# Optimization experiments

Hardware: AMD Instinct MI355X
Metric: run time of the kernel (lower is better)

## Reference

```python
import jax, jax.numpy as jnp
import numpy as np

NUM_USERS = 100000
NUM_ITEMS = 50000
NUM_NODES = NUM_USERS + NUM_ITEMS
EMBED_DIM = 128
NUM_LAYERS = 3
CONTENT_DIM = 768
NUM_EDGES = 1000000
BATCH = 4096
LAMBDA_CONTENT = 0.1
INIT_STD = 0.1


def setup_inputs() -> dict:
    key = jax.random.key(0)
    ks = jax.random.split(key, 9)
    edge_index = jax.random.randint(ks[0], (2, NUM_EDGES), 0, NUM_NODES, dtype=jnp.int64 if jax.config.jax_enable_x64 else jnp.int32)
    edge_weight = jax.random.uniform(ks[1], (NUM_EDGES,), dtype=jnp.float32)
    batch_users = jax.random.randint(ks[2], (BATCH,), 0, NUM_USERS)
    batch_pos_items = jax.random.randint(ks[3], (BATCH,), 0, NUM_ITEMS)
    batch_neg_items = jax.random.randint(ks[4], (BATCH,), 0, NUM_ITEMS)
    item_content = jax.random.normal(ks[5], (NUM_ITEMS, CONTENT_DIM), dtype=jnp.float32)
    user_emb_w = INIT_STD * jax.random.normal(ks[6], (NUM_USERS, EMBED_DIM), dtype=jnp.float32)
    item_emb_w = INIT_STD * jax.random.normal(ks[7], (NUM_ITEMS, EMBED_DIM), dtype=jnp.float32)
    # nn.Linear(item_content_dim, embed_dim, bias=False): weight [embed_dim, content_dim]
    bound = 1.0 / np.sqrt(CONTENT_DIM)
    content_proj_w = jax.random.uniform(ks[8], (EMBED_DIM, CONTENT_DIM), minval=-bound, maxval=bound, dtype=jnp.float32)
    return {
        'edge_index': edge_index, 'edge_weight': edge_weight,
        'batch_users': batch_users, 'batch_pos_items': batch_pos_items,
        'batch_neg_items': batch_neg_items, 'item_content': item_content,
        'user_emb_w': user_emb_w, 'item_emb_w': item_emb_w,
        'content_proj_w': content_proj_w,
    }


def _lgconv(x, src, dst, ew, num_nodes):
    # PyG LGConv: gcn_norm(add_self_loops=False) then scatter-add at target.
    deg = jax.ops.segment_sum(ew, dst, num_segments=num_nodes)          # [N]
    dinv = jnp.where(deg > 0, jax.lax.rsqrt(deg), 0.0)
    norm = dinv[src] * ew * dinv[dst]                                    # [E]
    return jax.ops.segment_sum(norm[:, None] * x[src], dst, num_segments=num_nodes)


def _propagate(user_emb_w, item_emb_w, src, dst, ew):
    x = jnp.concatenate([user_emb_w, item_emb_w], axis=0)               # [N, D]
    acc = x
    for _ in range(NUM_LAYERS):
        x = _lgconv(x, src, dst, ew, NUM_NODES)
        acc = acc + x
    x_final = acc / (NUM_LAYERS + 1)
    return x_final[:NUM_USERS], x_final[NUM_USERS:]


def reference(edge_index, edge_weight, batch_users, batch_pos_items,
              batch_neg_items, item_content, user_emb_w, item_emb_w,
              content_proj_w):
    src, dst = edge_index[0], edge_index[1]
    u_final, i_final = _propagate(user_emb_w, item_emb_w, src, dst, edge_weight)
    u = u_final[batch_users]
    i_pos = i_final[batch_pos_items]
    i_neg = i_final[batch_neg_items]
    pos_score = jnp.sum(u * i_pos, axis=-1)
    neg_score = jnp.sum(u * i_neg, axis=-1)
    bpr = jnp.mean(jax.nn.softplus(-(pos_score - neg_score)))
    reg = jnp.mean(jnp.sum(u**2, axis=1) + jnp.sum(i_pos**2, axis=1) + jnp.sum(i_neg**2, axis=1)) * 1e-4
    proj = item_content @ content_proj_w.T                              # [I, D]
    align = jnp.mean((i_final - proj) ** 2)
    loss = bpr + reg + LAMBDA_CONTENT * align
    return loss, u_final, i_final
```

## Files before the change

### kernel.cpp

```cpp
#include <hip/hip_runtime.h>
#include <math.h>

#define NU 100000
#define NI 50000
#define NN 150000
#define D 128
#define NE 1000000
#define CD 768
#define BATCH 4096

typedef short bf16x8 __attribute__((ext_vector_type(8)));
typedef float f32x4 __attribute__((ext_vector_type(4)));

static inline size_t alignup(size_t x, size_t a) { return (x + a - 1) / a * a; }

__device__ inline unsigned short f2bf(float f) {
  unsigned int u = __builtin_bit_cast(unsigned int, f);
  unsigned int r = (u + 0x7fffu + ((u >> 16) & 1u)) >> 16;
  return (unsigned short)r;
}
__device__ inline unsigned int pack2bf(float lo, float hi) {
  return (unsigned int)f2bf(lo) | ((unsigned int)f2bf(hi) << 16);
}
__device__ inline float bflo(unsigned int p) {
  return __builtin_bit_cast(float, p << 16);
}
__device__ inline float bfhi(unsigned int p) {
  return __builtin_bit_cast(float, p & 0xffff0000u);
}

__global__ __launch_bounds__(256) void prep_kernel(
    const int* __restrict__ dst, int* __restrict__ cnt, int* __restrict__ cpos,
    const float* __restrict__ uemb, const float* __restrict__ iemb,
    unsigned int* __restrict__ x0b,
    const float* __restrict__ W, unsigned short* __restrict__ Wb) {
  int half = blockIdx.x >> 1;
  if ((blockIdx.x & 1) == 0) {
    int i = half * 256 + threadIdx.x;
    for (; i < NE; i += 2048 * 256)
      cpos[i] = atomicAdd(&cnt[dst[i]], 1);
  } else {
    const size_t XT = (size_t)NN * D / 8;
    const size_t WT = (size_t)D * CD / 8;
    size_t t = (size_t)half * 256 + threadIdx.x;
    for (; t < XT + WT; t += (size_t)2048 * 256) {
      if (t < XT) {
        size_t f = t * 8;
        const float* p = (f < (size_t)NU * D) ? (uemb + f) : (iemb + (f - (size_t)NU * D));
        float4 a = *(const float4*)p;
        float4 b = *(const float4*)(p + 4);
        uint4 o;
        o.x = pack2bf(a.x, a.y); o.y = pack2bf(a.z, a.w);
        o.z = pack2bf(b.x, b.y); o.w = pack2bf(b.z, b.w);
        *(uint4*)(x0b + t * 4) = o;
      } else {
        size_t f = (t - XT) * 8;
        float4 a = *(const float4*)(W + f);
        float4 b = *(const float4*)(W + f + 4);
        uint4 o;
        o.x = (unsigned int)f2bf(a.x) | ((unsigned int)f2bf(a.y) << 16);
        o.y = (unsigned int)f2bf(a.z) | ((unsigned int)f2bf(a.w) << 16);
        o.z = (unsigned int)f2bf(b.x) | ((unsigned int)f2bf(b.y) << 16);
        o.w = (unsigned int)f2bf(b.z) | ((unsigned int)f2bf(b.w) << 16);
        *(uint4*)(Wb + f) = o;
      }
    }
  }
}


__global__ void scan_p1(const int* __restrict__ cnt, int* __restrict__ bsum) {
  __shared__ int s[256];
  int b = blockIdx.x;
  int i = b * 256 + threadIdx.x;
  s[threadIdx.x] = (i < NN) ? cnt[i] : 0;
  __syncthreads();
  for (int off = 128; off; off >>= 1) {
    if (threadIdx.x < off) s[threadIdx.x] += s[threadIdx.x + off];
    __syncthreads();
  }
  if (threadIdx.x == 0) bsum[b] = s[0];
}

__global__ __launch_bounds__(1024) void scan_p2(int* __restrict__ bsum, int nb) {
  __shared__ int s[1024];
  int t = threadIdx.x;
  int v = (t < nb) ? bsum[t] : 0;
  s[t] = v;
  __syncthreads();
  for (int off = 1; off < 1024; off <<= 1) {
    int u = (t >= off) ? s[t - off] : 0;
    __syncthreads();
    s[t] += u;
    __syncthreads();
  }
  if (t < nb) bsum[t] = s[t] - v;
}

__global__ void scan_p3(const int* __restrict__ cnt, const int* __restrict__ bsum,
                        int* __restrict__ row_ptr) {
  __shared__ int s[256];
  int b = blockIdx.x;
  int i = b * 256 + threadIdx.x;
  s[threadIdx.x] = (i < NN) ? cnt[i] : 0;
  __syncthreads();
  for (int off = 1; off < 256; off <<= 1) {
    int t = (threadIdx.x >= off) ? s[threadIdx.x - off] : 0;
    __syncthreads();
    s[threadIdx.x] += t;
    __syncthreads();
  }
  if (i < NN) row_ptr[i + 1] = bsum[b] + s[threadIdx.x];
  if (i == 0) row_ptr[0] = 0;
}

__global__ void fill_kernel(const int* __restrict__ src, const int* __restrict__ dst,
                            const float* __restrict__ ew, const int* __restrict__ row_ptr,
                            const int* __restrict__ cpos, int* __restrict__ csrc,
                            float* __restrict__ cew) {
  int i = blockIdx.x * blockDim.x + threadIdx.x;
  int stride = gridDim.x * blockDim.x;
  for (; i < NE; i += stride) {
    int p = row_ptr[dst[i]] + cpos[i];
    csrc[p] = src[i];
    cew[p] = ew[i];
  }
}

__global__ void degrow_kernel(const int* __restrict__ row_ptr, const float* __restrict__ cew,
                              float* __restrict__ dinv) {
  int n = blockIdx.x * blockDim.x + threadIdx.x;
  if (n >= NN) return;
  int beg = row_ptr[n], end = row_ptr[n + 1];
  float s = 0.f;
  for (int p = beg; p < end; ++p) s += cew[p];
  dinv[n] = (s > 0.f) ? rsqrtf(s) : 0.f;
}

__global__ void norm_kernel(const int* __restrict__ csrc, const float* __restrict__ cew,
                            const float* __restrict__ dinv, float* __restrict__ cnorm) {
  int i = blockIdx.x * blockDim.x + threadIdx.x;
  int stride = gridDim.x * blockDim.x;
  for (; i < NE; i += stride) cnorm[i] = dinv[csrc[i]] * cew[i];
}

#define GATHER_BODY(SRCBUF)                                                          \
  int tid = threadIdx.x;                                                             \
  int wv = tid >> 6, lane = tid & 63;                                                \
  int g = lane >> 4, sub = lane & 15;                                                \
  int n = blockIdx.x * 16 + wv * 4 + g;                                              \
  if (n >= NN) return;                                                               \
  int beg = row_ptr[n], end = row_ptr[n + 1];                                        \
  float a0 = 0.f, a1 = 0.f, a2 = 0.f, a3 = 0.f, a4 = 0.f, a5 = 0.f, a6 = 0.f, a7 = 0.f; \
  int j = beg;                                                                       \
  for (; j + 2 <= end; j += 2) {                                                     \
    int s0 = csrc[j], s1 = csrc[j + 1];                                              \
    float w0 = cnorm[j], w1 = cnorm[j + 1];                                          \
    uint4 p0 = SRCBUF[(size_t)s0 * 16 + sub];                                        \
    uint4 p1 = SRCBUF[(size_t)s1 * 16 + sub];                                        \
    a0 = fmaf(w0, bflo(p0.x), a0); a1 = fmaf(w0, bfhi(p0.x), a1);                    \
    a2 = fmaf(w0, bflo(p0.y), a2); a3 = fmaf(w0, bfhi(p0.y), a3);                    \
    a4 = fmaf(w0, bflo(p0.z), a4); a5 = fmaf(w0, bfhi(p0.z), a5);                    \
    a6 = fmaf(w0, bflo(p0.w), a6); a7 = fmaf(w0, bfhi(p0.w), a7);                    \
    a0 = fmaf(w1, bflo(p1.x), a0); a1 = fmaf(w1, bfhi(p1.x), a1);                    \
    a2 = fmaf(w1, bflo(p1.y), a2); a3 = fmaf(w1, bfhi(p1.y), a3);                    \
    a4 = fmaf(w1, bflo(p1.z), a4); a5 = fmaf(w1, bfhi(p1.z), a5);                    \
    a6 = fmaf(w1, bflo(p1.w), a6); a7 = fmaf(w1, bfhi(p1.w), a7);                    \
  }                                                                                  \
  if (j < end) {                                                                     \
    int s0 = csrc[j];                                                                \
    float w0 = cnorm[j];                                                             \
    uint4 p0 = SRCBUF[(size_t)s0 * 16 + sub];                                        \
    a0 = fmaf(w0, bflo(p0.x), a0); a1 = fmaf(w0, bfhi(p0.x), a1);                    \
    a2 = fmaf(w0, bflo(p0.y), a2); a3 = fmaf(w0, bfhi(p0.y), a3);                    \
    a4 = fmaf(w0, bflo(p0.z), a4); a5 = fmaf(w0, bfhi(p0.z), a5);                    \
    a6 = fmaf(w0, bflo(p0.w), a6); a7 = fmaf(w0, bfhi(p0.w), a7);                    \
  }

__global__ __launch_bounds__(256) void gather_kernel(
    const int* __restrict__ row_ptr, const int* __restrict__ csrc,
    const float* __restrict__ cnorm, const float* __restrict__ dinv,
    const uint4* __restrict__ xin, uint4* __restrict__ yout) {
  GATHER_BODY(xin)
  float sc = dinv[n];
  uint4 o;
  o.x = pack2bf(a0 * sc, a1 * sc);
  o.y = pack2bf(a2 * sc, a3 * sc);
  o.z = pack2bf(a4 * sc, a5 * sc);
  o.w = pack2bf(a6 * sc, a7 * sc);
  yout[(size_t)n * 16 + sub] = o;
}

__global__ __launch_bounds__(256) void final_kernel(
    const int* __restrict__ row_ptr, const int* __restrict__ csrc,
    const float* __restrict__ cnorm, const float* __restrict__ dinv,
    const uint4* __restrict__ x0b, const uint4* __restrict__ y1b,
    const uint4* __restrict__ y2b, float* __restrict__ OUT) {
  GATHER_BODY(y2b)
  float sc = dinv[n];
  size_t r = (size_t)n * 16 + sub;
  uint4 q0 = x0b[r], q1 = y1b[r], q2 = y2b[r];
  float* op = OUT + (size_t)n * D + sub * 8;
  op[0] = (bflo(q0.x) + bflo(q1.x) + bflo(q2.x) + a0 * sc) * 0.25f;
  op[1] = (bfhi(q0.x) + bfhi(q1.x) + bfhi(q2.x) + a1 * sc) * 0.25f;
  op[2] = (bflo(q0.y) + bflo(q1.y) + bflo(q2.y) + a2 * sc) * 0.25f;
  op[3] = (bfhi(q0.y) + bfhi(q1.y) + bfhi(q2.y) + a3 * sc) * 0.25f;
  op[4] = (bflo(q0.z) + bflo(q1.z) + bflo(q2.z) + a4 * sc) * 0.25f;
  op[5] = (bfhi(q0.z) + bfhi(q1.z) + bfhi(q2.z) + a5 * sc) * 0.25f;
  op[6] = (bflo(q0.w) + bflo(q1.w) + bflo(q2.w) + a6 * sc) * 0.25f;
  op[7] = (bfhi(q0.w) + bfhi(q1.w) + bfhi(q2.w) + a7 * sc) * 0.25f;
}

__global__ __launch_bounds__(512) void align_mfma_kernel(
    const float* __restrict__ content, const unsigned short* __restrict__ Wb,
    const float* __restrict__ ifinal, float* __restrict__ accums) {
  __shared__ unsigned short Asm[2][64 * 64];
  __shared__ unsigned short Bsm[2][128 * 64];
  __shared__ float wred[8];

  int tid = threadIdx.x;
  int w = tid >> 6, lane = tid & 63;
  int i0 = blockIdx.x * 64;
  int lrow = lane & 15, kq = lane >> 4;

  f32x4 acc[4];
#pragma unroll
  for (int rt = 0; rt < 4; ++rt) acc[rt] = (f32x4){0.f, 0.f, 0.f, 0.f};

  int sr = tid >> 3, c8 = tid & 7;
  int arow_g = (i0 + sr < NI) ? (i0 + sr) : (NI - 1);
  const float* aG = content + (size_t)arow_g * CD + c8 * 8;
  const unsigned short* bG0 = Wb + (size_t)sr * CD + c8 * 8;
  const unsigned short* bG1 = Wb + (size_t)(sr + 64) * CD + c8 * 8;
  int aoff = (c8 * 16) ^ ((sr & 7) << 4);
  int boff0 = aoff;
  int boff1 = (c8 * 16) ^ (((sr + 64) & 7) << 4);

  {
    float4 a = *(const float4*)(aG);
    float4 b = *(const float4*)(aG + 4);
    uint4 o;
    o.x = pack2bf(a.x, a.y); o.y = pack2bf(a.z, a.w);
    o.z = pack2bf(b.x, b.y); o.w = pack2bf(b.z, b.w);
    *(uint4*)((char*)Asm[0] + sr * 128 + aoff) = o;
    *(uint4*)((char*)Bsm[0] + sr * 128 + boff0) = *(const uint4*)(bG0);
    *(uint4*)((char*)Bsm[0] + (sr + 64) * 128 + boff1) = *(const uint4*)(bG1);
  }

  for (int kk = 0; kk < 6; ++kk) {
    __syncthreads();
    int cur = kk & 1, nxt = cur ^ 1;
    bool more = kk < 5;
    float4 na, nb;
    uint4 nb0, nb1;
    if (more) {
      int k0 = (kk + 1) * 64;
      na = *(const float4*)(aG + k0);
      nb = *(const float4*)(aG + k0 + 4);
      nb0 = *(const uint4*)(bG0 + k0);
      nb1 = *(const uint4*)(bG1 + k0);
    }
#pragma unroll
    for (int ks = 0; ks < 2; ++ks) {
      int kbyte = ks * 64 + kq * 16;
      bf16x8 af[4], bfr;
#pragma unroll
      for (int rt = 0; rt < 4; ++rt) {
        int row = rt * 16 + lrow;
        af[rt] = *(const bf16x8*)((char*)Asm[cur] + row * 128 + (kbyte ^ ((row & 7) << 4)));
      }
      {
        int row = w * 16 + lrow;
        bfr = *(const bf16x8*)((char*)Bsm[cur] + row * 128 + (kbyte ^ ((row & 7) << 4)));
      }
#pragma unroll
      for (int rt = 0; rt < 4; ++rt)
        acc[rt] = __builtin_amdgcn_mfma_f32_16x16x32_bf16(af[rt], bfr, acc[rt], 0, 0, 0);
    }
    if (more) {
      uint4 o;
      o.x = pack2bf(na.x, na.y); o.y = pack2bf(na.z, na.w);
      o.z = pack2bf(nb.x, nb.y); o.w = pack2bf(nb.z, nb.w);
      *(uint4*)((char*)Asm[nxt] + sr * 128 + aoff) = o;
      *(uint4*)((char*)Bsm[nxt] + sr * 128 + boff0) = nb0;
      *(uint4*)((char*)Bsm[nxt] + (sr + 64) * 128 + boff1) = nb1;
    }
  }

  float s = 0.f;
  int dcol = w * 16 + lrow;
#pragma unroll
  for (int rt = 0; rt < 4; ++rt) {
#pragma unroll
    for (int j = 0; j < 4; ++j) {
      int it = i0 + rt * 16 + kq * 4 + j;
      if (it < NI) {
        float r0 = ifinal[(size_t)it * D + dcol];
        float d0 = r0 - acc[rt][j];
        s = fmaf(d0, d0, s);
      }
    }
  }
  for (int off = 32; off; off >>= 1) s += __shfl_down(s, off);
  if (lane == 0) wred[w] = s;
  __syncthreads();
  if (tid == 0) {
    float t = 0.f;
#pragma unroll
    for (int q = 0; q < 8; ++q) t += wred[q];
    atomicAdd(&accums[2], t);
  }
}

__global__ __launch_bounds__(256) void loss_batch(
    const int* __restrict__ bu, const int* __restrict__ bp, const int* __restrict__ bn,
    const float* __restrict__ OUT, float* __restrict__ accums) {
  __shared__ float wsp[4], wrg[4];
  int wv = threadIdx.x >> 6, lane = threadIdx.x & 63;
  int gw = blockIdx.x * 4 + wv;
  int nw = gridDim.x * 4;
  float lsp = 0.f, lrg = 0.f;
  for (int b = gw; b < BATCH; b += nw) {
    const float* u = OUT + (size_t)bu[b] * D;
    const float* ip = OUT + ((size_t)NU + bp[b]) * D;
    const float* in_ = OUT + ((size_t)NU + bn[b]) * D;
    float u0 = u[lane], u1 = u[lane + 64];
    float p0 = ip[lane], p1 = ip[lane + 64];
    float n0 = in_[lane], n1 = in_[lane + 64];
    float ps = u0 * p0 + u1 * p1;
    float ns = u0 * n0 + u1 * n1;
    float rg = u0 * u0 + u1 * u1 + p0 * p0 + p1 * p1 + n0 * n0 + n1 * n1;
    for (int off = 32; off; off >>= 1) {
      ps += __shfl_down(ps, off);
      ns += __shfl_down(ns, off);
      rg += __shfl_down(rg, off);
    }
    if (lane == 0) {
      float x = ns - ps;
      lsp += fmaxf(x, 0.f) + log1pf(expf(-fabsf(x)));
      lrg += rg;
    }
  }
  if (lane == 0) { wsp[wv] = lsp; wrg[wv] = lrg; }
  __syncthreads();
  if (threadIdx.x == 0) {
    atomicAdd(&accums[0], wsp[0] + wsp[1] + wsp[2] + wsp[3]);
    atomicAdd(&accums[1], wrg[0] + wrg[1] + wrg[2] + wrg[3]);
  }
}

__global__ void finalize_kernel(const float* __restrict__ accums, float* __restrict__ out0) {
  if (threadIdx.x == 0 && blockIdx.x == 0) {
    float bpr = accums[0] / (float)BATCH;
    float reg = (accums[1] / (float)BATCH) * 1e-4f;
    float align = accums[2] / (float)((size_t)NI * D);
    out0[0] = bpr + reg + 0.1f * align;
  }
}

extern "C" void kernel_launch(void* const* d_in, const int* in_sizes, int n_in,
                              void* d_out, int out_size, void* d_ws, size_t ws_size,
                              hipStream_t stream) {
  const int* edge_index = (const int*)d_in[0];
  const float* ew = (const float*)d_in[1];
  const int* bu = (const int*)d_in[2];
  const int* bp = (const int*)d_in[3];
  const int* bn = (const int*)d_in[4];
  const float* content = (const float*)d_in[5];
  const float* uemb = (const float*)d_in[6];
  const float* iemb = (const float*)d_in[7];
  const float* W = (const float*)d_in[8];
  const int* src = edge_index;
  const int* dst = edge_index + NE;
  float* outf = (float*)d_out;
  float* OUT = outf + 1;

  char* ws = (char*)d_ws;
  size_t off = 0;
  auto alloc = [&](size_t bytes) {
    void* p = ws + off;
    off = alignup(off + bytes, 256);
    return p;
  };
  unsigned int* x0b = (unsigned int*)alloc((size_t)NN * 64 * 4);
  unsigned int* y1b = (unsigned int*)alloc((size_t)NN * 64 * 4);
  unsigned int* y2b = (unsigned int*)alloc((size_t)NN * 64 * 4);
  float* dinv = (float*)alloc((size_t)NN * 4);
  int* cnt = (int*)alloc((size_t)NN * 4);
  int* row_ptr = (int*)alloc((size_t)(NN + 1) * 4);
  int NB = (NN + 255) / 256;
  int* bsum = (int*)alloc((size_t)NB * 4);
  int* cpos = (int*)alloc((size_t)NE * 4);
  int* csrc = (int*)alloc((size_t)NE * 4);
  float* cew = (float*)alloc((size_t)NE * 4);
  float* cnorm = (float*)alloc((size_t)NE * 4);
  unsigned short* Wb = (unsigned short*)alloc((size_t)D * CD * 2);
  float* accums = (float*)alloc(16);

  hipMemsetAsync(cnt, 0, (size_t)NN * 4, stream);
  hipMemsetAsync(accums, 0, 16, stream);

  prep_kernel<<<4096, 256, 0, stream>>>(dst, cnt, cpos, uemb, iemb, x0b, W, Wb);
  scan_p1<<<NB, 256, 0, stream>>>(cnt, bsum);
  scan_p2<<<1, 1024, 0, stream>>>(bsum, NB);
  scan_p3<<<NB, 256, 0, stream>>>(cnt, bsum, row_ptr);
  fill_kernel<<<2048, 256, 0, stream>>>(src, dst, ew, row_ptr, cpos, csrc, cew);
  degrow_kernel<<<NB, 256, 0, stream>>>(row_ptr, cew, dinv);
  norm_kernel<<<2048, 256, 0, stream>>>(csrc, cew, dinv, cnorm);

  int LB = (NN + 15) / 16;
  gather_kernel<<<LB, 256, 0, stream>>>(row_ptr, csrc, cnorm, dinv, (const uint4*)x0b, (uint4*)y1b);
  gather_kernel<<<LB, 256, 0, stream>>>(row_ptr, csrc, cnorm, dinv, (const uint4*)y1b, (uint4*)y2b);
  final_kernel<<<LB, 256, 0, stream>>>(row_ptr, csrc, cnorm, dinv,
                                       (const uint4*)x0b, (const uint4*)y1b, (const uint4*)y2b, OUT);

  align_mfma_kernel<<<(NI + 63) / 64, 512, 0, stream>>>(content, Wb, OUT + (size_t)NU * D, accums);
  loss_batch<<<64, 256, 0, stream>>>(bu, bp, bn, OUT, accums);
  finalize_kernel<<<1, 64, 0, stream>>>(accums, outf);
}
```

Before: 341.9 us.

## Fuse content projection GEMM into prep kernel and alignment loss into final gather

Moves the content-projection MFMA GEMM into the prep kernel as extra blocks, so it runs alongside the counting and bf16 conversion work, and writes the projection to a bf16 buffer. The alignment MSE is then computed inside the final gather kernel, which removes the separate align kernel and its re-read of i_final. Partial sums go to 256 slots that a wider finalize kernel reduces. In exchange, the bf16 projection buffer adds a write and read plus extra rounding, and W is now converted to bf16 inside every GEMM block.

```diff
diff --git a/kernel.cpp b/kernel.cpp
--- a/kernel.cpp
+++ b/kernel.cpp
@@ -8,6 +8,7 @@
 #define NE 1000000
 #define CD 768
 #define BATCH 4096
+#define NGEMM 782
 
 typedef short bf16x8 __attribute__((ext_vector_type(8)));
 typedef float f32x4 __attribute__((ext_vector_type(4)));
@@ -29,22 +30,29 @@
   return __builtin_bit_cast(float, p & 0xffff0000u);
 }
 
-__global__ __launch_bounds__(256) void prep_kernel(
+__global__ __launch_bounds__(512) void prep_kernel(
     const int* __restrict__ dst, int* __restrict__ cnt, int* __restrict__ cpos,
     const float* __restrict__ uemb, const float* __restrict__ iemb,
     unsigned int* __restrict__ x0b,
-    const float* __restrict__ W, unsigned short* __restrict__ Wb) {
-  int half = blockIdx.x >> 1;
-  if ((blockIdx.x & 1) == 0) {
-    int i = half * 256 + threadIdx.x;
-    for (; i < NE; i += 2048 * 256)
-      cpos[i] = atomicAdd(&cnt[dst[i]], 1);
-  } else {
-    const size_t XT = (size_t)NN * D / 8;
-    const size_t WT = (size_t)D * CD / 8;
-    size_t t = (size_t)half * 256 + threadIdx.x;
-    for (; t < XT + WT; t += (size_t)2048 * 256) {
-      if (t < XT) {
+    const float* __restrict__ W, const float* __restrict__ content,
+    uint4* __restrict__ proj) {
+  __shared__ unsigned short Asm[2][64 * 64];
+  __shared__ unsigned short Bsm[2][128 * 64];
+
+  int bid = blockIdx.x;
+  int tid = threadIdx.x;
+
+  if (bid >= NGEMM) {
+    int sub = bid - NGEMM;
+    int half = sub >> 1;
+    if ((sub & 1) == 0) {
+      int i = half * 512 + tid;
+      for (; i < NE; i += 1024 * 512)
+        cpos[i] = atomicAdd(&cnt[dst[i]], 1);
+    } else {
+      const size_t XT = (size_t)NN * D / 8;
+      size_t t = (size_t)half * 512 + tid;
+      for (; t < XT; t += (size_t)1024 * 512) {
         size_t f = t * 8;
         const float* p = (f < (size_t)NU * D) ? (uemb + f) : (iemb + (f - (size_t)NU * D));
         float4 a = *(const float4*)p;
@@ -53,18 +61,107 @@
         o.x = pack2bf(a.x, a.y); o.y = pack2bf(a.z, a.w);
         o.z = pack2bf(b.x, b.y); o.w = pack2bf(b.z, b.w);
         *(uint4*)(x0b + t * 4) = o;
-      } else {
-        size_t f = (t - XT) * 8;
-        float4 a = *(const float4*)(W + f);
-        float4 b = *(const float4*)(W + f + 4);
-        uint4 o;
-        o.x = (unsigned int)f2bf(a.x) | ((unsigned int)f2bf(a.y) << 16);
-        o.y = (unsigned int)f2bf(a.z) | ((unsigned int)f2bf(a.w) << 16);
-        o.z = (unsigned int)f2bf(b.x) | ((unsigned int)f2bf(b.y) << 16);
-        o.w = (unsigned int)f2bf(b.z) | ((unsigned int)f2bf(b.w) << 16);
-        *(uint4*)(Wb + f) = o;
       }
     }
+    return;
+  }
+
+  int w = tid >> 6, lane = tid & 63;
+  int i0 = bid * 64;
+  int lrow = lane & 15, kq = lane >> 4;
+
+  f32x4 acc[4];
+#pragma unroll
+  for (int rt = 0; rt < 4; ++rt) acc[rt] = (f32x4){0.f, 0.f, 0.f, 0.f};
+
+  int sr = tid >> 3, c8 = tid & 7;
+  int arow_g = (i0 + sr < NI) ? (i0 + sr) : (NI - 1);
+  const float* aG = content + (size_t)arow_g * CD + c8 * 8;
+  const float* bG0 = W + (size_t)sr * CD + c8 * 8;
+  const float* bG1 = W + (size_t)(sr + 64) * CD + c8 * 8;
+  int aoff = (c8 * 16) ^ ((sr & 7) << 4);
+  int boff0 = aoff;
+  int boff1 = (c8 * 16) ^ (((sr + 64) & 7) << 4);
+
+  {
+    float4 a0 = *(const float4*)(aG);
+    float4 a1 = *(const float4*)(aG + 4);
+    float4 p0 = *(const float4*)(bG0);
+    float4 p1 = *(const float4*)(bG0 + 4);
+    float4 q0 = *(const float4*)(bG1);
+    float4 q1 = *(const float4*)(bG1 + 4);
+    uint4 oa, ob, oc;
+    oa.x = pack2bf(a0.x, a0.y); oa.y = pack2bf(a0.z, a0.w);
+    oa.z = pack2bf(a1.x, a1.y); oa.w = pack2bf(a1.z, a1.w);
+    ob.x = pack2bf(p0.x, p0.y); ob.y = pack2bf(p0.z, p0.w);
+    ob.z = pack2bf(p1.x, p1.y); ob.w = pack2bf(p1.z, p1.w);
+    oc.x = pack2bf(q0.x, q0.y); oc.y = pack2bf(q0.z, q0.w);
+    oc.z = pack2bf(q1.x, q1.y); oc.w = pack2bf(q1.z, q1.w);
+    *(uint4*)((char*)Asm[0] + sr * 128 + aoff) = oa;
+    *(uint4*)((char*)Bsm[0] + sr * 128 + boff0) = ob;
+    *(uint4*)((char*)Bsm[0] + (sr + 64) * 128 + boff1) = oc;
+  }
+
+  for (int kk = 0; kk < 6; ++kk) {
+    __syncthreads();
+    int cur = kk & 1, nxt = cur ^ 1;
+    bool more = kk < 5;
+    float4 a0, a1, p0, p1, q0, q1;
+    if (more) {
+      int k0 = (kk + 1) * 64;
+      a0 = *(const float4*)(aG + k0);
+      a1 = *(const float4*)(aG + k0 + 4);
+      p0 = *(const float4*)(bG0 + k0);
+      p1 = *(const float4*)(bG0 + k0 + 4);
+      q0 = *(const float4*)(bG1 + k0);
+      q1 = *(const float4*)(bG1 + k0 + 4);
+    }
+#pragma unroll
+    for (int ks = 0; ks < 2; ++ks) {
+      int kbyte = ks * 64 + kq * 16;
+      bf16x8 af[4], bfr;
+#pragma unroll
+      for (int rt = 0; rt < 4; ++rt) {
+        int row = rt * 16 + lrow;
+        af[rt] = *(const bf16x8*)((char*)Asm[cur] + row * 128 + (kbyte ^ ((row & 7) << 4)));
+      }
+      {
+        int row = w * 16 + lrow;
+        bfr = *(const bf16x8*)((char*)Bsm[cur] + row * 128 + (kbyte ^ ((row & 7) << 4)));
+      }
+#pragma unroll
+      for (int rt = 0; rt < 4; ++rt)
+        acc[rt] = __builtin_amdgcn_mfma_f32_16x16x32_bf16(af[rt], bfr, acc[rt], 0, 0, 0);
+    }
+    if (more) {
+      uint4 oa, ob, oc;
+      oa.x = pack2bf(a0.x, a0.y); oa.y = pack2bf(a0.z, a0.w);
+      oa.z = pack2bf(a1.x, a1.y); oa.w = pack2bf(a1.z, a1.w);
+      ob.x = pack2bf(p0.x, p0.y); ob.y = pack2bf(p0.z, p0.w);
+      ob.z = pack2bf(p1.x, p1.y); ob.w = pack2bf(p1.z, p1.w);
+      oc.x = pack2bf(q0.x, q0.y); oc.y = pack2bf(q0.z, q0.w);
+      oc.z = pack2bf(q1.x, q1.y); oc.w = pack2bf(q1.z, q1.w);
+      *(uint4*)((char*)Asm[nxt] + sr * 128 + aoff) = oa;
+      *(uint4*)((char*)Bsm[nxt] + sr * 128 + boff0) = ob;
+      *(uint4*)((char*)Bsm[nxt] + (sr + 64) * 128 + boff1) = oc;
+    }
+  }
+
+  __syncthreads();
+  unsigned short* T = (unsigned short*)Asm;
+  int dcol = w * 16 + lrow;
+#pragma unroll
+  for (int rt = 0; rt < 4; ++rt)
+#pragma unroll
+    for (int j = 0; j < 4; ++j)
+      T[(rt * 16 + kq * 4 + j) * 128 + dcol] = f2bf(acc[rt][j]);
+  __syncthreads();
+#pragma unroll
+  for (int u0 = 0; u0 < 2; ++u0) {
+    int u = u0 * 512 + tid;
+    int r = u >> 4, s = u & 15;
+    int it = i0 + r;
+    if (it < NI) proj[(size_t)it * 16 + s] = ((const uint4*)T)[u];
   }
 }
 
@@ -195,120 +292,38 @@
     const int* __restrict__ row_ptr, const int* __restrict__ csrc,
     const float* __restrict__ cnorm, const float* __restrict__ dinv,
     const uint4* __restrict__ x0b, const uint4* __restrict__ y1b,
-    const uint4* __restrict__ y2b, float* __restrict__ OUT) {
+    const uint4* __restrict__ y2b, const uint4* __restrict__ proj,
+    float* __restrict__ OUT, float* __restrict__ partials) {
+  __shared__ float wred[4];
   GATHER_BODY(y2b)
   float sc = dinv[n];
   size_t r = (size_t)n * 16 + sub;
   uint4 q0 = x0b[r], q1 = y1b[r], q2 = y2b[r];
+  float v[8];
+  v[0] = (bflo(q0.x) + bflo(q1.x) + bflo(q2.x) + a0 * sc) * 0.25f;
+  v[1] = (bfhi(q0.x) + bfhi(q1.x) + bfhi(q2.x) + a1 * sc) * 0.25f;
+  v[2] = (bflo(q0.y) + bflo(q1.y) + bflo(q2.y) + a2 * sc) * 0.25f;
+  v[3] = (bfhi(q0.y) + bfhi(q1.y) + bfhi(q2.y) + a3 * sc) * 0.25f;
+  v[4] = (bflo(q0.z) + bflo(q1.z) + bflo(q2.z) + a4 * sc) * 0.25f;
+  v[5] = (bfhi(q0.z) + bfhi(q1.z) + bfhi(q2.z) + a5 * sc) * 0.25f;
+  v[6] = (bflo(q0.w) + bflo(q1.w) + bflo(q2.w) + a6 * sc) * 0.25f;
+  v[7] = (bfhi(q0.w) + bfhi(q1.w) + bfhi(q2.w) + a7 * sc) * 0.25f;
   float* op = OUT + (size_t)n * D + sub * 8;
-  op[0] = (bflo(q0.x) + bflo(q1.x) + bflo(q2.x) + a0 * sc) * 0.25f;
-  op[1] = (bfhi(q0.x) + bfhi(q1.x) + bfhi(q2.x) + a1 * sc) * 0.25f;
-  op[2] = (bflo(q0.y) + bflo(q1.y) + bflo(q2.y) + a2 * sc) * 0.25f;
-  op[3] = (bfhi(q0.y) + bfhi(q1.y) + bfhi(q2.y) + a3 * sc) * 0.25f;
-  op[4] = (bflo(q0.z) + bflo(q1.z) + bflo(q2.z) + a4 * sc) * 0.25f;
-  op[5] = (bfhi(q0.z) + bfhi(q1.z) + bfhi(q2.z) + a5 * sc) * 0.25f;
-  op[6] = (bflo(q0.w) + bflo(q1.w) + bflo(q2.w) + a6 * sc) * 0.25f;
-  op[7] = (bfhi(q0.w) + bfhi(q1.w) + bfhi(q2.w) + a7 * sc) * 0.25f;
-}
-
-__global__ __launch_bounds__(512) void align_mfma_kernel(
-    const float* __restrict__ content, const unsigned short* __restrict__ Wb,
-    const float* __restrict__ ifinal, float* __restrict__ accums) {
-  __shared__ unsigned short Asm[2][64 * 64];
-  __shared__ unsigned short Bsm[2][128 * 64];
-  __shared__ float wred[8];
-
-  int tid = threadIdx.x;
-  int w = tid >> 6, lane = tid & 63;
-  int i0 = blockIdx.x * 64;
-  int lrow = lane & 15, kq = lane >> 4;
-
-  f32x4 acc[4];
-#pragma unroll
-  for (int rt = 0; rt < 4; ++rt) acc[rt] = (f32x4){0.f, 0.f, 0.f, 0.f};
-
-  int sr = tid >> 3, c8 = tid & 7;
-  int arow_g = (i0 + sr < NI) ? (i0 + sr) : (NI - 1);
-  const float* aG = content + (size_t)arow_g * CD + c8 * 8;
-  const unsigned short* bG0 = Wb + (size_t)sr * CD + c8 * 8;
-  const unsigned short* bG1 = Wb + (size_t)(sr + 64) * CD + c8 * 8;
-  int aoff = (c8 * 16) ^ ((sr & 7) << 4);
-  int boff0 = aoff;
-  int boff1 = (c8 * 16) ^ (((sr + 64) & 7) << 4);
-
-  {
-    float4 a = *(const float4*)(aG);
-    float4 b = *(const float4*)(aG + 4);
-    uint4 o;
-    o.x = pack2bf(a.x, a.y); o.y = pack2bf(a.z, a.w);
-    o.z = pack2bf(b.x, b.y); o.w = pack2bf(b.z, b.w);
-    *(uint4*)((char*)Asm[0] + sr * 128 + aoff) = o;
-    *(uint4*)((char*)Bsm[0] + sr * 128 + boff0) = *(const uint4*)(bG0);
-    *(uint4*)((char*)Bsm[0] + (sr + 64) * 128 + boff1) = *(const uint4*)(bG1);
-  }
-
-  for (int kk = 0; kk < 6; ++kk) {
-    __syncthreads();
-    int cur = kk & 1, nxt = cur ^ 1;
-    bool more = kk < 5;
-    float4 na, nb;
-    uint4 nb0, nb1;
-    if (more) {
-      int k0 = (kk + 1) * 64;
-      na = *(const float4*)(aG + k0);
-      nb = *(const float4*)(aG + k0 + 4);
-      nb0 = *(const uint4*)(bG0 + k0);
-      nb1 = *(const uint4*)(bG1 + k0);
-    }
-#pragma unroll
-    for (int ks = 0; ks < 2; ++ks) {
-      int kbyte = ks * 64 + kq * 16;
-      bf16x8 af[4], bfr;
-#pragma unroll
-      for (int rt = 0; rt < 4; ++rt) {
-        int row = rt * 16 + lrow;
-        af[rt] = *(const bf16x8*)((char*)Asm[cur] + row * 128 + (kbyte ^ ((row & 7) << 4)));
-      }
-      {
-        int row = w * 16 + lrow;
-        bfr = *(const bf16x8*)((char*)Bsm[cur] + row * 128 + (kbyte ^ ((row & 7) << 4)));
-      }
-#pragma unroll
-      for (int rt = 0; rt < 4; ++rt)
-        acc[rt] = __builtin_amdgcn_mfma_f32_16x16x32_bf16(af[rt], bfr, acc[rt], 0, 0, 0);
-    }
-    if (more) {
-      uint4 o;
-      o.x = pack2bf(na.x, na.y); o.y = pack2bf(na.z, na.w);
-      o.z = pack2bf(nb.x, nb.y); o.w = pack2bf(nb.z, nb.w);
-      *(uint4*)((char*)Asm[nxt] + sr * 128 + aoff) = o;
-      *(uint4*)((char*)Bsm[nxt] + sr * 128 + boff0) = nb0;
-      *(uint4*)((char*)Bsm[nxt] + (sr + 64) * 128 + boff1) = nb1;
-    }
-  }
-
-  float s = 0.f;
-  int dcol = w * 16 + lrow;
-#pragma unroll
-  for (int rt = 0; rt < 4; ++rt) {
-#pragma unroll
-    for (int j = 0; j < 4; ++j) {
-      int it = i0 + rt * 16 + kq * 4 + j;
-      if (it < NI) {
-        float r0 = ifinal[(size_t)it * D + dcol];
-        float d0 = r0 - acc[rt][j];
-        s = fmaf(d0, d0, s);
-      }
-    }
-  }
-  for (int off = 32; off; off >>= 1) s += __shfl_down(s, off);
-  if (lane == 0) wred[w] = s;
-  __syncthreads();
-  if (tid == 0) {
-    float t = 0.f;
-#pragma unroll
-    for (int q = 0; q < 8; ++q) t += wred[q];
-    atomicAdd(&accums[2], t);
+#pragma unroll
+  for (int k = 0; k < 8; ++k) op[k] = v[k];
+
+  if (blockIdx.x >= (NU / 16)) {
+    uint4 pj = proj[(size_t)(n - NU) * 16 + sub];
+    float d0 = v[0] - bflo(pj.x), d1 = v[1] - bfhi(pj.x);
+    float d2 = v[2] - bflo(pj.y), d3 = v[3] - bfhi(pj.y);
+    float d4 = v[4] - bflo(pj.z), d5 = v[5] - bfhi(pj.z);
+    float d6 = v[6] - bflo(pj.w), d7 = v[7] - bfhi(pj.w);
+    float m = d0 * d0 + d1 * d1 + d2 * d2 + d3 * d3 + d4 * d4 + d5 * d5 + d6 * d6 + d7 * d7;
+    for (int off = 32; off; off >>= 1) m += __shfl_down(m, off);
+    if (lane == 0) wred[wv] = m;
+    __syncthreads();
+    if (tid == 0)
+      atomicAdd(&partials[blockIdx.x & 255], wred[0] + wred[1] + wred[2] + wred[3]);
   }
 }
 
@@ -349,11 +364,20 @@
   }
 }
 
-__global__ void finalize_kernel(const float* __restrict__ accums, float* __restrict__ out0) {
-  if (threadIdx.x == 0 && blockIdx.x == 0) {
+__global__ void finalize_kernel(const float* __restrict__ accums,
+                                const float* __restrict__ partials,
+                                float* __restrict__ out0) {
+  __shared__ float sm[4];
+  int tid = threadIdx.x;
+  float v = partials[tid];
+  for (int off = 32; off; off >>= 1) v += __shfl_down(v, off);
+  if ((tid & 63) == 0) sm[tid >> 6] = v;
+  __syncthreads();
+  if (tid == 0) {
+    float align_sum = sm[0] + sm[1] + sm[2] + sm[3];
     float bpr = accums[0] / (float)BATCH;
     float reg = (accums[1] / (float)BATCH) * 1e-4f;
-    float align = accums[2] / (float)((size_t)NI * D);
+    float align = align_sum / (float)((size_t)NI * D);
     out0[0] = bpr + reg + 0.1f * align;
   }
 }
@@ -385,6 +409,7 @@
   unsigned int* x0b = (unsigned int*)alloc((size_t)NN * 64 * 4);
   unsigned int* y1b = (unsigned int*)alloc((size_t)NN * 64 * 4);
   unsigned int* y2b = (unsigned int*)alloc((size_t)NN * 64 * 4);
+  uint4* proj = (uint4*)alloc((size_t)NI * 16 * 16);
   float* dinv = (float*)alloc((size_t)NN * 4);
   int* cnt = (int*)alloc((size_t)NN * 4);
   int* row_ptr = (int*)alloc((size_t)(NN + 1) * 4);
@@ -394,13 +419,13 @@
   int* csrc = (int*)alloc((size_t)NE * 4);
   float* cew = (float*)alloc((size_t)NE * 4);
   float* cnorm = (float*)alloc((size_t)NE * 4);
-  unsigned short* Wb = (unsigned short*)alloc((size_t)D * CD * 2);
-  float* accums = (float*)alloc(16);
+  float* accums = (float*)alloc(16 + 256 * 4);
+  float* partials = accums + 4;
 
   hipMemsetAsync(cnt, 0, (size_t)NN * 4, stream);
-  hipMemsetAsync(accums, 0, 16, stream);
-
-  prep_kernel<<<4096, 256, 0, stream>>>(dst, cnt, cpos, uemb, iemb, x0b, W, Wb);
+  hipMemsetAsync(accums, 0, 16 + 256 * 4, stream);
+
+  prep_kernel<<<NGEMM + 2048, 512, 0, stream>>>(dst, cnt, cpos, uemb, iemb, x0b, W, content, proj);
   scan_p1<<<NB, 256, 0, stream>>>(cnt, bsum);
   scan_p2<<<1, 1024, 0, stream>>>(bsum, NB);
   scan_p3<<<NB, 256, 0, stream>>>(cnt, bsum, row_ptr);
@@ -412,9 +437,9 @@
   gather_kernel<<<LB, 256, 0, stream>>>(row_ptr, csrc, cnorm, dinv, (const uint4*)x0b, (uint4*)y1b);
   gather_kernel<<<LB, 256, 0, stream>>>(row_ptr, csrc, cnorm, dinv, (const uint4*)y1b, (uint4*)y2b);
   final_kernel<<<LB, 256, 0, stream>>>(row_ptr, csrc, cnorm, dinv,
-                                       (const uint4*)x0b, (const uint4*)y1b, (const uint4*)y2b, OUT);
-
-  align_mfma_kernel<<<(NI + 63) / 64, 512, 0, stream>>>(content, Wb, OUT + (size_t)NU * D, accums);
+                                       (const uint4*)x0b, (const uint4*)y1b, (const uint4*)y2b,
+                                       proj, OUT, partials);
+
   loss_batch<<<64, 256, 0, stream>>>(bu, bp, bn, OUT, accums);
-  finalize_kernel<<<1, 64, 0, stream>>>(accums, outf);
-}
+  finalize_kernel<<<1, 256, 0, stream>>>(accums, partials, outf);
+}
```

Measured after the change: 324.8 us. 5.0% less time.
